# Performance work log

Hardware: AMD Instinct MI355X
Metric: run time of the kernel (lower is better)

Reference implementation:

```python
import jax, jax.numpy as jnp
import numpy as np

B, N, D, H = 32, 64, 128, 256

def setup_inputs() -> dict:
    key = jax.random.key(0)
    ks = jax.random.split(key, 6)
    s = 0.02
    return {
        "objects": jax.random.normal(ks[0], (B, N, D), dtype=jnp.float32),
        "gW1": jax.random.normal(ks[1], (2 * D, H), dtype=jnp.float32) * s,
        "gb1": jnp.zeros((H,), dtype=jnp.float32),
        "gW2": jax.random.normal(ks[2], (H, H), dtype=jnp.float32) * s,
        "gb2": jnp.zeros((H,), dtype=jnp.float32),
        "gW3": jax.random.normal(ks[3], (H, H), dtype=jnp.float32) * s,
        "gb3": jnp.zeros((H,), dtype=jnp.float32),
        "fW1": jax.random.normal(ks[4], (H, H), dtype=jnp.float32) * s,
        "fb1": jnp.zeros((H,), dtype=jnp.float32),
        "fW2": jax.random.normal(ks[5], (H, H), dtype=jnp.float32) * s,
        "fb2": jnp.zeros((H,), dtype=jnp.float32),
    }

def reference(objects, gW1, gb1, gW2, gb2, gW3, gb3, fW1, fb1, fW2, fb2):
    b, n, d = objects.shape
    # Pairwise concat: pair[b,i,j] = [objects[b,i], objects[b,j]] -> (B,N,N,2D)
    left = jnp.broadcast_to(objects[:, :, None, :], (b, n, n, d))
    right = jnp.broadcast_to(objects[:, None, :, :], (b, n, n, d))
    pair = jnp.concatenate([left, right], axis=-1)
    # g_theta: 3-layer MLP with ReLU after first two layers
    h = jax.nn.relu(pair @ gW1 + gb1)
    h = jax.nn.relu(h @ gW2 + gb2)
    h = h @ gW3 + gb3                      # (B,N,N,H)
    # Sum over all pairs i != j
    mask = (1.0 - jnp.eye(n, dtype=h.dtype))  # (N,N)
    agg = jnp.einsum('bijh,ij->bh', h, mask)  # (B,H)
    # f_phi: Linear-ReLU-Linear
    out = jax.nn.relu(agg @ fW1 + fb1) @ fW2 + fb2
    return out
```

## Files before the change

### kernel.cpp

```cpp
#include <hip/hip_runtime.h>
#include <hip/hip_bf16.h>

typedef __attribute__((ext_vector_type(8))) _Float16 half8;
typedef __attribute__((ext_vector_type(4))) float f32x4;

__global__ __launch_bounds__(256) void rn_prep(
    const float* __restrict__ obj, const float* __restrict__ gW1,
    const float* __restrict__ gb1, const float* __restrict__ gW2,
    _Float16* __restrict__ Lh, char* __restrict__ RhB,
    _Float16* __restrict__ W2h, float* __restrict__ S)
{
    __shared__ float so[8 * 128];
    __shared__ float tt[64 * 65];
    const int blk = blockIdx.x, t = threadIdx.x;

    if (blk < 256) {
        const int r0 = blk * 8;
        #pragma unroll
        for (int it = 0; it < 4; ++it) so[it * 256 + t] = obj[r0 * 128 + it * 256 + t];
        __syncthreads();
        float accL[8], accR[8];
        #pragma unroll
        for (int r = 0; r < 8; ++r) { accL[r] = 0.f; accR[r] = 0.f; }
        for (int k = 0; k < 128; ++k) {
            float wL = gW1[k * 256 + t];
            float wR = gW1[(128 + k) * 256 + t];
            #pragma unroll
            for (int r = 0; r < 8; ++r) {
                float o = so[r * 128 + k];
                accL[r] += o * wL;
                accR[r] += o * wR;
            }
        }
        float bb = gb1[t];
        #pragma unroll
        for (int r = 0; r < 8; ++r) {
            int row = r0 + r;
            Lh[row * 256 + t] = (_Float16)(accL[r] + bb);
            *(_Float16*)(RhB + row * 512 + ((2 * t) ^ ((row & 15) << 4))) = (_Float16)accR[r];
        }
    } else if (blk < 272) {
        const int tb = blk - 256;
        const int k0 = (tb >> 2) * 64, c0 = (tb & 3) * 64;
        for (int it = 0; it < 16; ++it) {
            int idx = it * 256 + t, rr = idx >> 6, cc = idx & 63;
            tt[rr * 65 + cc] = gW2[(k0 + rr) * 256 + c0 + cc];
        }
        __syncthreads();
        for (int it = 0; it < 16; ++it) {
            int idx = it * 256 + t, cr = idx >> 6, kk = idx & 63;
            W2h[(c0 + cr) * 256 + (k0 + kk)] = (_Float16)tt[kk * 65 + cr];
        }
    } else {
        for (int it = 0; it < 32; ++it) S[it * 256 + t] = 0.f;
    }
}

__global__ __launch_bounds__(512, 2) void rn_main(
    const char* __restrict__ LhB, const char* __restrict__ RhB,
    const _Float16* __restrict__ W2h, const float* __restrict__ gb2,
    float* __restrict__ S)
{
    __shared__ __attribute__((aligned(16))) char smem[36864];
    const int blk = blockIdx.x;
    const int b = blk >> 3, ig = blk & 7;
    const int t = threadIdx.x, lane = t & 63, w = t >> 6;
    const int mg = w >> 2, ng = w & 3;
    const int lc = lane & 15, lg = lane >> 4;

    {
        const char* gR = RhB + b * 32768;
        #pragma unroll
        for (int it = 0; it < 4; ++it) {
            int u = it * 512 + t;
            *(f32x4*)(smem + u * 16) = *(const f32x4*)(gR + u * 16);
        }
        if (t < 256) {
            const char* gL = LhB + (b * 64 + ig * 8) * 512;
            *(f32x4*)(smem + 32768 + t * 16) = *(const f32x4*)(gL + t * 16);
        }
    }

    half8 bfr[4][8];
    #pragma unroll
    for (int n = 0; n < 4; ++n)
        #pragma unroll
        for (int ks = 0; ks < 8; ++ks)
            bfr[n][ks] = *(const half8*)(W2h + (ng * 64 + n * 16 + lc) * 256 + ks * 32 + lg * 8);

    float bias[4];
    #pragma unroll
    for (int n = 0; n < 4; ++n) bias[n] = gb2[ng * 64 + n * 16 + lc];

    __syncthreads();

    half8 rh[2][8];
    #pragma unroll
    for (int m2 = 0; m2 < 2; ++m2) {
        int row = mg * 32 + m2 * 16 + lc;
        #pragma unroll
        for (int ks = 0; ks < 8; ++ks) {
            int kb = ks * 64 + lg * 16;
            rh[m2][ks] = *(const half8*)(smem + row * 512 + (kb ^ (lc << 4)));
        }
    }

    const half8 zero8 = {(_Float16)0.f, (_Float16)0.f, (_Float16)0.f, (_Float16)0.f,
                         (_Float16)0.f, (_Float16)0.f, (_Float16)0.f, (_Float16)0.f};
    float csum[4] = {0.f, 0.f, 0.f, 0.f};

    for (int ii = 0; ii < 8; ++ii) {
        f32x4 acc[2][4];
        #pragma unroll
        for (int m2 = 0; m2 < 2; ++m2)
            #pragma unroll
            for (int n = 0; n < 4; ++n)
                acc[m2][n] = (f32x4){0.f, 0.f, 0.f, 0.f};

        #pragma unroll
        for (int ks = 0; ks < 8; ++ks) {
            half8 lhv = *(const half8*)(smem + 32768 + ii * 512 + ks * 64 + lg * 16);
            #pragma unroll
            for (int m2 = 0; m2 < 2; ++m2) {
                half8 av = lhv + rh[m2][ks];
                av = __builtin_elementwise_max(av, zero8);
                #pragma unroll
                for (int n = 0; n < 4; ++n)
                    acc[m2][n] = __builtin_amdgcn_mfma_f32_16x16x32_f16(
                        av, bfr[n][ks], acc[m2][n], 0, 0, 0);
            }
        }

        const int iglob = ig * 8 + ii;
        #pragma unroll
        for (int n = 0; n < 4; ++n) {
            float cs = 0.f;
            #pragma unroll
            for (int m2 = 0; m2 < 2; ++m2)
                #pragma unroll
                for (int q = 0; q < 4; ++q) {
                    int row = mg * 32 + m2 * 16 + lg * 4 + q;
                    float v = fmaxf(acc[m2][n][q] + bias[n], 0.f);
                    cs += (row == iglob) ? 0.f : v;
                }
            csum[n] += cs;
        }
    }

    #pragma unroll
    for (int n = 0; n < 4; ++n) {
        float cs = csum[n];
        cs += __shfl_xor(cs, 16);
        cs += __shfl_xor(cs, 32);
        if (lane < 16) atomicAdd(&S[b * 256 + ng * 64 + n * 16 + lc], cs);
    }
}

__global__ __launch_bounds__(1024) void rn_final(
    const float* __restrict__ S, const float* __restrict__ gW3,
    const float* __restrict__ gb3, const float* __restrict__ fW1,
    const float* __restrict__ fb1, const float* __restrict__ fW2,
    const float* __restrict__ fb2, float* __restrict__ out)
{
    __shared__ float vec[256];
    __shared__ float ps[16][260];
    const int b = blockIdx.x, t = threadIdx.x;
    const int cg = t & 63, kq = t >> 6;
    const int c0 = cg * 4;

    if (t < 256) vec[t] = S[b * 256 + t];
    __syncthreads();

    {
        f32x4 s = (f32x4){0.f, 0.f, 0.f, 0.f};
        #pragma unroll
        for (int kk = 0; kk < 16; ++kk) {
            int k = kq * 16 + kk;
            f32x4 wv = *(const f32x4*)&gW3[k * 256 + c0];
            s += wv * vec[k];
        }
        *(f32x4*)&ps[kq][c0] = s;
    }
    __syncthreads();
    if (t < 256) {
        float a = 0.f;
        #pragma unroll
        for (int q = 0; q < 16; ++q) a += ps[q][t];
        vec[t] = a + 4032.0f * gb3[t];
    }
    __syncthreads();

    {
        f32x4 s = (f32x4){0.f, 0.f, 0.f, 0.f};
        #pragma unroll
        for (int kk = 0; kk < 16; ++kk) {
            int k = kq * 16 + kk;
            f32x4 wv = *(const f32x4*)&fW1[k * 256 + c0];
            s += wv * vec[k];
        }
        *(f32x4*)&ps[kq][c0] = s;
    }
    __syncthreads();
    if (t < 256) {
        float a = 0.f;
        #pragma unroll
        for (int q = 0; q < 16; ++q) a += ps[q][t];
        vec[t] = fmaxf(a + fb1[t], 0.f);
    }
    __syncthreads();

    {
        f32x4 s = (f32x4){0.f, 0.f, 0.f, 0.f};
        #pragma unroll
        for (int kk = 0; kk < 16; ++kk) {
            int k = kq * 16 + kk;
            f32x4 wv = *(const f32x4*)&fW2[k * 256 + c0];
            s += wv * vec[k];
        }
        *(f32x4*)&ps[kq][c0] = s;
    }
    __syncthreads();
    if (t < 256) {
        float a = 0.f;
        #pragma unroll
        for (int q = 0; q < 16; ++q) a += ps[q][t];
        out[b * 256 + t] = a + fb2[t];
    }
}

extern "C" void kernel_launch(void* const* d_in, const int* in_sizes, int n_in,
                              void* d_out, int out_size, void* d_ws, size_t ws_size,
                              hipStream_t stream)
{
    const float* obj = (const float*)d_in[0];
    const float* gW1 = (const float*)d_in[1];
    const float* gb1 = (const float*)d_in[2];
    const float* gW2 = (const float*)d_in[3];
    const float* gb2 = (const float*)d_in[4];
    const float* gW3 = (const float*)d_in[5];
    const float* gb3 = (const float*)d_in[6];
    const float* fW1 = (const float*)d_in[7];
    const float* fb1 = (const float*)d_in[8];
    const float* fW2 = (const float*)d_in[9];
    const float* fb2 = (const float*)d_in[10];
    float* out = (float*)d_out;

    char* ws = (char*)d_ws;
    _Float16* Lh  = (_Float16*)(ws);
    char*     RhB = ws + (1u << 20);
    _Float16* W2h = (_Float16*)(ws + (2u << 20));
    float*    S   = (float*)(ws + (2u << 20) + (128u << 10));

    rn_prep <<<273, 256, 0, stream>>>(obj, gW1, gb1, gW2, Lh, RhB, W2h, S);
    rn_main <<<256, 512, 0, stream>>>((const char*)Lh, RhB, W2h, gb2, S);
    rn_final<<<32, 1024, 0, stream>>>(S, gW3, gb3, fW1, fb1, fW2, fb2, out);
}
```

Before: 44.47 us.

## Fuse final MLP into main kernel via last-block-per-batch atomic counter

Removes the separate rn_final launch. Each rn_main block bumps a per-batch counter after its atomic adds, and the last of the 8 blocks for a batch runs the gW3/f_phi tail with 512 threads instead of 1024. The W2 fragment register loads are also hoisted ahead of the shared-memory staging to overlap global latency. This saves one kernel launch and its gap, but the tail now runs serially at the end of the last block and needs a counter reset in prep plus fences.

```diff
diff --git a/kernel.cpp b/kernel.cpp
--- a/kernel.cpp
+++ b/kernel.cpp
@@ -8,7 +8,7 @@
     const float* __restrict__ obj, const float* __restrict__ gW1,
     const float* __restrict__ gb1, const float* __restrict__ gW2,
     _Float16* __restrict__ Lh, char* __restrict__ RhB,
-    _Float16* __restrict__ W2h, float* __restrict__ S)
+    _Float16* __restrict__ W2h, float* __restrict__ S, int* __restrict__ cnt)
 {
     __shared__ float so[8 * 128];
     __shared__ float tt[64 * 65];
@@ -53,21 +53,34 @@
         }
     } else {
         for (int it = 0; it < 32; ++it) S[it * 256 + t] = 0.f;
+        if (t < 32) cnt[t] = 0;
     }
 }
 
 __global__ __launch_bounds__(512, 2) void rn_main(
     const char* __restrict__ LhB, const char* __restrict__ RhB,
     const _Float16* __restrict__ W2h, const float* __restrict__ gb2,
-    float* __restrict__ S)
+    float* __restrict__ S, int* __restrict__ cnt,
+    const float* __restrict__ gW3, const float* __restrict__ gb3,
+    const float* __restrict__ fW1, const float* __restrict__ fb1,
+    const float* __restrict__ fW2, const float* __restrict__ fb2,
+    float* __restrict__ out)
 {
     __shared__ __attribute__((aligned(16))) char smem[36864];
+    __shared__ int lastFlag;
     const int blk = blockIdx.x;
     const int b = blk >> 3, ig = blk & 7;
     const int t = threadIdx.x, lane = t & 63, w = t >> 6;
     const int mg = w >> 2, ng = w & 3;
     const int lc = lane & 15, lg = lane >> 4;
 
+    half8 bfr[4][8];
+    #pragma unroll
+    for (int n = 0; n < 4; ++n)
+        #pragma unroll
+        for (int ks = 0; ks < 8; ++ks)
+            bfr[n][ks] = *(const half8*)(W2h + (ng * 64 + n * 16 + lc) * 256 + ks * 32 + lg * 8);
+
     {
         const char* gR = RhB + b * 32768;
         #pragma unroll
@@ -80,13 +93,6 @@
             *(f32x4*)(smem + 32768 + t * 16) = *(const f32x4*)(gL + t * 16);
         }
     }
-
-    half8 bfr[4][8];
-    #pragma unroll
-    for (int n = 0; n < 4; ++n)
-        #pragma unroll
-        for (int ks = 0; ks < 8; ++ks)
-            bfr[n][ks] = *(const half8*)(W2h + (ng * 64 + n * 16 + lc) * 256 + ks * 32 + lg * 8);
 
     float bias[4];
     #pragma unroll
@@ -154,30 +160,33 @@
         cs += __shfl_xor(cs, 32);
         if (lane < 16) atomicAdd(&S[b * 256 + ng * 64 + n * 16 + lc], cs);
     }
-}
-
-__global__ __launch_bounds__(1024) void rn_final(
-    const float* __restrict__ S, const float* __restrict__ gW3,
-    const float* __restrict__ gb3, const float* __restrict__ fW1,
-    const float* __restrict__ fb1, const float* __restrict__ fW2,
-    const float* __restrict__ fb2, float* __restrict__ out)
-{
-    __shared__ float vec[256];
-    __shared__ float ps[16][260];
-    const int b = blockIdx.x, t = threadIdx.x;
+
+    __threadfence();
+    __syncthreads();
+    if (t == 0) {
+        int old = __hip_atomic_fetch_add(&cnt[b], 1, __ATOMIC_ACQ_REL,
+                                         __HIP_MEMORY_SCOPE_AGENT);
+        lastFlag = (old == 7);
+    }
+    __syncthreads();
+    if (!lastFlag) return;
+
+    float* vec = (float*)smem;
+    float (*ps)[260] = (float(*)[260])(smem + 2048);
+    if (t < 256)
+        vec[t] = __hip_atomic_load(&S[b * 256 + t], __ATOMIC_RELAXED,
+                                   __HIP_MEMORY_SCOPE_AGENT);
+    __syncthreads();
+
     const int cg = t & 63, kq = t >> 6;
     const int c0 = cg * 4;
 
-    if (t < 256) vec[t] = S[b * 256 + t];
-    __syncthreads();
-
     {
         f32x4 s = (f32x4){0.f, 0.f, 0.f, 0.f};
         #pragma unroll
-        for (int kk = 0; kk < 16; ++kk) {
-            int k = kq * 16 + kk;
-            f32x4 wv = *(const f32x4*)&gW3[k * 256 + c0];
-            s += wv * vec[k];
+        for (int kk = 0; kk < 32; ++kk) {
+            int k = kq * 32 + kk;
+            s += (*(const f32x4*)&gW3[k * 256 + c0]) * vec[k];
         }
         *(f32x4*)&ps[kq][c0] = s;
     }
@@ -185,7 +194,7 @@
     if (t < 256) {
         float a = 0.f;
         #pragma unroll
-        for (int q = 0; q < 16; ++q) a += ps[q][t];
+        for (int q = 0; q < 8; ++q) a += ps[q][t];
         vec[t] = a + 4032.0f * gb3[t];
     }
     __syncthreads();
@@ -193,10 +202,9 @@
     {
         f32x4 s = (f32x4){0.f, 0.f, 0.f, 0.f};
         #pragma unroll
-        for (int kk = 0; kk < 16; ++kk) {
-            int k = kq * 16 + kk;
-            f32x4 wv = *(const f32x4*)&fW1[k * 256 + c0];
-            s += wv * vec[k];
+        for (int kk = 0; kk < 32; ++kk) {
+            int k = kq * 32 + kk;
+            s += (*(const f32x4*)&fW1[k * 256 + c0]) * vec[k];
         }
         *(f32x4*)&ps[kq][c0] = s;
     }
@@ -204,7 +212,7 @@
     if (t < 256) {
         float a = 0.f;
         #pragma unroll
-        for (int q = 0; q < 16; ++q) a += ps[q][t];
+        for (int q = 0; q < 8; ++q) a += ps[q][t];
         vec[t] = fmaxf(a + fb1[t], 0.f);
     }
     __syncthreads();
@@ -212,10 +220,9 @@
     {
         f32x4 s = (f32x4){0.f, 0.f, 0.f, 0.f};
         #pragma unroll
-        for (int kk = 0; kk < 16; ++kk) {
-            int k = kq * 16 + kk;
-            f32x4 wv = *(const f32x4*)&fW2[k * 256 + c0];
-            s += wv * vec[k];
+        for (int kk = 0; kk < 32; ++kk) {
+            int k = kq * 32 + kk;
+            s += (*(const f32x4*)&fW2[k * 256 + c0]) * vec[k];
         }
         *(f32x4*)&ps[kq][c0] = s;
     }
@@ -223,7 +230,7 @@
     if (t < 256) {
         float a = 0.f;
         #pragma unroll
-        for (int q = 0; q < 16; ++q) a += ps[q][t];
+        for (int q = 0; q < 8; ++q) a += ps[q][t];
         out[b * 256 + t] = a + fb2[t];
     }
 }
@@ -250,8 +257,9 @@
     char*     RhB = ws + (1u << 20);
     _Float16* W2h = (_Float16*)(ws + (2u << 20));
     float*    S   = (float*)(ws + (2u << 20) + (128u << 10));
-
-    rn_prep <<<273, 256, 0, stream>>>(obj, gW1, gb1, gW2, Lh, RhB, W2h, S);
-    rn_main <<<256, 512, 0, stream>>>((const char*)Lh, RhB, W2h, gb2, S);
-    rn_final<<<32, 1024, 0, stream>>>(S, gW3, gb3, fW1, fb1, fW2, fb2, out);
+    int*      cnt = (int*)(ws + (2u << 20) + (160u << 10));
+
+    rn_prep <<<273, 256, 0, stream>>>(obj, gW1, gb1, gW2, Lh, RhB, W2h, S, cnt);
+    rn_main <<<256, 512, 0, stream>>>((const char*)Lh, RhB, W2h, gb2, S, cnt,
+                                      gW3, gb3, fW1, fb1, fW2, fb2, out);
 }
```

Result: slower. 70.94 us (+59.5%).

## Precompute gW3·fW1 product in prep kernel to drop a GEMV stage from final kernel

Applied to the files above, without the earlier changes.

The final layer gW3 and the first f_phi layer are linear back to back, so the prep kernel now builds M = gW3 @ fW1 and a folded bias vector (4032*gb3@fW1 + fb1). That lets rn_final skip one matrix-vector stage and its barriers. fW2 is also prefetched into registers early to hide its load latency. The cost is 32 extra prep blocks doing a 256x256x256 fp32 GEMM every call, plus one bias block with a serial 256-term loop. That work runs in parallel with the existing prep blocks but could lengthen the prep kernel.

```diff
diff --git a/kernel.cpp b/kernel.cpp
--- a/kernel.cpp
+++ b/kernel.cpp
@@ -7,11 +7,15 @@
 __global__ __launch_bounds__(256) void rn_prep(
     const float* __restrict__ obj, const float* __restrict__ gW1,
     const float* __restrict__ gb1, const float* __restrict__ gW2,
+    const float* __restrict__ gW3, const float* __restrict__ gb3,
+    const float* __restrict__ fW1, const float* __restrict__ fb1,
     _Float16* __restrict__ Lh, char* __restrict__ RhB,
-    _Float16* __restrict__ W2h, float* __restrict__ S)
+    _Float16* __restrict__ W2h, float* __restrict__ S,
+    float* __restrict__ M, float* __restrict__ dvec)
 {
     __shared__ float so[8 * 128];
     __shared__ float tt[64 * 65];
+    __shared__ float sg[8][256];
     const int blk = blockIdx.x, t = threadIdx.x;
 
     if (blk < 256) {
@@ -51,8 +55,26 @@
             int idx = it * 256 + t, cr = idx >> 6, kk = idx & 63;
             W2h[(c0 + cr) * 256 + (k0 + kk)] = (_Float16)tt[kk * 65 + cr];
         }
+    } else if (blk == 272) {
+        for (int it = 0; it < 32; ++it) S[it * 256 + t] = 0.f;
+        float a = 0.f;
+        for (int j = 0; j < 256; ++j) a += gb3[j] * fW1[j * 256 + t];
+        dvec[t] = 4032.0f * a + fb1[t];
     } else {
-        for (int it = 0; it < 32; ++it) S[it * 256 + t] = 0.f;
+        const int r0 = (blk - 273) * 8;
+        #pragma unroll
+        for (int it = 0; it < 8; ++it) sg[it][t] = gW3[(r0 + it) * 256 + t];
+        __syncthreads();
+        float acc[8];
+        #pragma unroll
+        for (int r = 0; r < 8; ++r) acc[r] = 0.f;
+        for (int j = 0; j < 256; ++j) {
+            float wv = fW1[j * 256 + t];
+            #pragma unroll
+            for (int r = 0; r < 8; ++r) acc[r] += sg[r][j] * wv;
+        }
+        #pragma unroll
+        for (int r = 0; r < 8; ++r) M[(r0 + r) * 256 + t] = acc[r];
     }
 }
 
@@ -157,9 +179,8 @@
 }
 
 __global__ __launch_bounds__(1024) void rn_final(
-    const float* __restrict__ S, const float* __restrict__ gW3,
-    const float* __restrict__ gb3, const float* __restrict__ fW1,
-    const float* __restrict__ fb1, const float* __restrict__ fW2,
+    const float* __restrict__ S, const float* __restrict__ M,
+    const float* __restrict__ dvec, const float* __restrict__ fW2,
     const float* __restrict__ fb2, float* __restrict__ out)
 {
     __shared__ float vec[256];
@@ -171,52 +192,33 @@
     if (t < 256) vec[t] = S[b * 256 + t];
     __syncthreads();
 
+    f32x4 w2r[16];
     {
         f32x4 s = (f32x4){0.f, 0.f, 0.f, 0.f};
         #pragma unroll
         for (int kk = 0; kk < 16; ++kk) {
             int k = kq * 16 + kk;
-            f32x4 wv = *(const f32x4*)&gW3[k * 256 + c0];
-            s += wv * vec[k];
+            s += (*(const f32x4*)&M[k * 256 + c0]) * vec[k];
         }
         *(f32x4*)&ps[kq][c0] = s;
+        #pragma unroll
+        for (int kk = 0; kk < 16; ++kk)
+            w2r[kk] = *(const f32x4*)&fW2[(kq * 16 + kk) * 256 + c0];
     }
     __syncthreads();
     if (t < 256) {
         float a = 0.f;
         #pragma unroll
         for (int q = 0; q < 16; ++q) a += ps[q][t];
-        vec[t] = a + 4032.0f * gb3[t];
+        vec[t] = fmaxf(a + dvec[t], 0.f);
     }
     __syncthreads();
 
     {
         f32x4 s = (f32x4){0.f, 0.f, 0.f, 0.f};
         #pragma unroll
-        for (int kk = 0; kk < 16; ++kk) {
-            int k = kq * 16 + kk;
-            f32x4 wv = *(const f32x4*)&fW1[k * 256 + c0];
-            s += wv * vec[k];
-        }
-        *(f32x4*)&ps[kq][c0] = s;
-    }
-    __syncthreads();
-    if (t < 256) {
-        float a = 0.f;
-        #pragma unroll
-        for (int q = 0; q < 16; ++q) a += ps[q][t];
-        vec[t] = fmaxf(a + fb1[t], 0.f);
-    }
-    __syncthreads();
-
-    {
-        f32x4 s = (f32x4){0.f, 0.f, 0.f, 0.f};
-        #pragma unroll
-        for (int kk = 0; kk < 16; ++kk) {
-            int k = kq * 16 + kk;
-            f32x4 wv = *(const f32x4*)&fW2[k * 256 + c0];
-            s += wv * vec[k];
-        }
+        for (int kk = 0; kk < 16; ++kk)
+            s += w2r[kk] * vec[kq * 16 + kk];
         *(f32x4*)&ps[kq][c0] = s;
     }
     __syncthreads();
@@ -250,8 +252,11 @@
     char*     RhB = ws + (1u << 20);
     _Float16* W2h = (_Float16*)(ws + (2u << 20));
     float*    S   = (float*)(ws + (2u << 20) + (128u << 10));
-
-    rn_prep <<<273, 256, 0, stream>>>(obj, gW1, gb1, gW2, Lh, RhB, W2h, S);
+    float*    M   = (float*)(ws + (2u << 20) + (160u << 10));
+    float*    dv  = (float*)(ws + (2u << 20) + (416u << 10));
+
+    rn_prep <<<305, 256, 0, stream>>>(obj, gW1, gb1, gW2, gW3, gb3, fW1, fb1,
+                                      Lh, RhB, W2h, S, M, dv);
     rn_main <<<256, 512, 0, stream>>>((const char*)Lh, RhB, W2h, gb2, S);
-    rn_final<<<32, 1024, 0, stream>>>(S, gW3, gb3, fW1, fb1, fW2, fb2, out);
-}
+    rn_final<<<32, 1024, 0, stream>>>(S, M, dv, fW2, fb2, out);
+}
```

Result: slower. 47.95 us (+7.8%).

## Split rn_main output columns across two blocks with 1024 threads each

Applied to the files above, without the earlier changes.

Reworks the main pairwise kernel so each block handles half of the 256 output columns, with 16 waves each owning one 16-row tile and two 16-column tiles. The grid doubles to 512 blocks of 1024 threads, cutting per-thread register state (fewer B fragments and accumulators) and giving more waves to hide latency. The cost is that each block still loads the full R tile and L rows, so shared-memory fill traffic doubles, and the ReLU-add of the A operand is now recomputed per column half. The rn_final edits are cosmetic.

```diff
diff --git a/kernel.cpp b/kernel.cpp
--- a/kernel.cpp
+++ b/kernel.cpp
@@ -56,23 +56,35 @@
     }
 }
 
-__global__ __launch_bounds__(512, 2) void rn_main(
+__global__ __launch_bounds__(1024) void rn_main(
     const char* __restrict__ LhB, const char* __restrict__ RhB,
     const _Float16* __restrict__ W2h, const float* __restrict__ gb2,
     float* __restrict__ S)
 {
     __shared__ __attribute__((aligned(16))) char smem[36864];
     const int blk = blockIdx.x;
-    const int b = blk >> 3, ig = blk & 7;
+    const int b = blk >> 4, ig = (blk >> 1) & 7, half = blk & 1;
     const int t = threadIdx.x, lane = t & 63, w = t >> 6;
-    const int mg = w >> 2, ng = w & 3;
+    const int mr = w & 3, nc = w >> 2;
     const int lc = lane & 15, lg = lane >> 4;
 
+    half8 bfr[2][8];
+    #pragma unroll
+    for (int n = 0; n < 2; ++n)
+        #pragma unroll
+        for (int ks = 0; ks < 8; ++ks)
+            bfr[n][ks] = *(const half8*)(W2h +
+                (half * 128 + nc * 32 + n * 16 + lc) * 256 + ks * 32 + lg * 8);
+
+    float bias[2];
+    #pragma unroll
+    for (int n = 0; n < 2; ++n) bias[n] = gb2[half * 128 + nc * 32 + n * 16 + lc];
+
     {
         const char* gR = RhB + b * 32768;
         #pragma unroll
-        for (int it = 0; it < 4; ++it) {
-            int u = it * 512 + t;
+        for (int it = 0; it < 2; ++it) {
+            int u = it * 1024 + t;
             *(f32x4*)(smem + u * 16) = *(const f32x4*)(gR + u * 16);
         }
         if (t < 256) {
@@ -80,79 +92,53 @@
             *(f32x4*)(smem + 32768 + t * 16) = *(const f32x4*)(gL + t * 16);
         }
     }
-
-    half8 bfr[4][8];
-    #pragma unroll
-    for (int n = 0; n < 4; ++n)
-        #pragma unroll
-        for (int ks = 0; ks < 8; ++ks)
-            bfr[n][ks] = *(const half8*)(W2h + (ng * 64 + n * 16 + lc) * 256 + ks * 32 + lg * 8);
-
-    float bias[4];
-    #pragma unroll
-    for (int n = 0; n < 4; ++n) bias[n] = gb2[ng * 64 + n * 16 + lc];
-
-    __syncthreads();
-
-    half8 rh[2][8];
-    #pragma unroll
-    for (int m2 = 0; m2 < 2; ++m2) {
-        int row = mg * 32 + m2 * 16 + lc;
+    __syncthreads();
+
+    half8 rh[8];
+    {
+        int row = mr * 16 + lc;
         #pragma unroll
         for (int ks = 0; ks < 8; ++ks) {
             int kb = ks * 64 + lg * 16;
-            rh[m2][ks] = *(const half8*)(smem + row * 512 + (kb ^ (lc << 4)));
+            rh[ks] = *(const half8*)(smem + row * 512 + (kb ^ (lc << 4)));
         }
     }
 
     const half8 zero8 = {(_Float16)0.f, (_Float16)0.f, (_Float16)0.f, (_Float16)0.f,
                          (_Float16)0.f, (_Float16)0.f, (_Float16)0.f, (_Float16)0.f};
-    float csum[4] = {0.f, 0.f, 0.f, 0.f};
-
+    float csum[2] = {0.f, 0.f};
+
+    #pragma unroll 1
     for (int ii = 0; ii < 8; ++ii) {
-        f32x4 acc[2][4];
-        #pragma unroll
-        for (int m2 = 0; m2 < 2; ++m2)
-            #pragma unroll
-            for (int n = 0; n < 4; ++n)
-                acc[m2][n] = (f32x4){0.f, 0.f, 0.f, 0.f};
+        f32x4 acc0 = (f32x4){0.f, 0.f, 0.f, 0.f};
+        f32x4 acc1 = (f32x4){0.f, 0.f, 0.f, 0.f};
 
         #pragma unroll
         for (int ks = 0; ks < 8; ++ks) {
             half8 lhv = *(const half8*)(smem + 32768 + ii * 512 + ks * 64 + lg * 16);
-            #pragma unroll
-            for (int m2 = 0; m2 < 2; ++m2) {
-                half8 av = lhv + rh[m2][ks];
-                av = __builtin_elementwise_max(av, zero8);
-                #pragma unroll
-                for (int n = 0; n < 4; ++n)
-                    acc[m2][n] = __builtin_amdgcn_mfma_f32_16x16x32_f16(
-                        av, bfr[n][ks], acc[m2][n], 0, 0, 0);
-            }
+            half8 av = __builtin_elementwise_max(lhv + rh[ks], zero8);
+            acc0 = __builtin_amdgcn_mfma_f32_16x16x32_f16(av, bfr[0][ks], acc0, 0, 0, 0);
+            acc1 = __builtin_amdgcn_mfma_f32_16x16x32_f16(av, bfr[1][ks], acc1, 0, 0, 0);
         }
 
         const int iglob = ig * 8 + ii;
         #pragma unroll
-        for (int n = 0; n < 4; ++n) {
-            float cs = 0.f;
-            #pragma unroll
-            for (int m2 = 0; m2 < 2; ++m2)
-                #pragma unroll
-                for (int q = 0; q < 4; ++q) {
-                    int row = mg * 32 + m2 * 16 + lg * 4 + q;
-                    float v = fmaxf(acc[m2][n][q] + bias[n], 0.f);
-                    cs += (row == iglob) ? 0.f : v;
-                }
-            csum[n] += cs;
+        for (int q = 0; q < 4; ++q) {
+            int row = mr * 16 + lg * 4 + q;
+            float v0 = fmaxf(acc0[q] + bias[0], 0.f);
+            float v1 = fmaxf(acc1[q] + bias[1], 0.f);
+            csum[0] += (row == iglob) ? 0.f : v0;
+            csum[1] += (row == iglob) ? 0.f : v1;
         }
     }
 
     #pragma unroll
-    for (int n = 0; n < 4; ++n) {
+    for (int n = 0; n < 2; ++n) {
         float cs = csum[n];
         cs += __shfl_xor(cs, 16);
         cs += __shfl_xor(cs, 32);
-        if (lane < 16) atomicAdd(&S[b * 256 + ng * 64 + n * 16 + lc], cs);
+        if (lane < 16)
+            atomicAdd(&S[b * 256 + half * 128 + nc * 32 + n * 16 + lc], cs);
     }
 }
 
@@ -176,8 +162,7 @@
         #pragma unroll
         for (int kk = 0; kk < 16; ++kk) {
             int k = kq * 16 + kk;
-            f32x4 wv = *(const f32x4*)&gW3[k * 256 + c0];
-            s += wv * vec[k];
+            s += (*(const f32x4*)&gW3[k * 256 + c0]) * vec[k];
         }
         *(f32x4*)&ps[kq][c0] = s;
     }
@@ -195,8 +180,7 @@
         #pragma unroll
         for (int kk = 0; kk < 16; ++kk) {
             int k = kq * 16 + kk;
-            f32x4 wv = *(const f32x4*)&fW1[k * 256 + c0];
-            s += wv * vec[k];
+            s += (*(const f32x4*)&fW1[k * 256 + c0]) * vec[k];
         }
         *(f32x4*)&ps[kq][c0] = s;
     }
@@ -214,8 +198,7 @@
         #pragma unroll
         for (int kk = 0; kk < 16; ++kk) {
             int k = kq * 16 + kk;
-            f32x4 wv = *(const f32x4*)&fW2[k * 256 + c0];
-            s += wv * vec[k];
+            s += (*(const f32x4*)&fW2[k * 256 + c0]) * vec[k];
         }
         *(f32x4*)&ps[kq][c0] = s;
     }
@@ -252,6 +235,6 @@
     float*    S   = (float*)(ws + (2u << 20) + (128u << 10));
 
     rn_prep <<<273, 256, 0, stream>>>(obj, gW1, gb1, gW2, Lh, RhB, W2h, S);
-    rn_main <<<256, 512, 0, stream>>>((const char*)Lh, RhB, W2h, gb2, S);
+    rn_main <<<512, 1024, 0, stream>>>((const char*)Lh, RhB, W2h, gb2, S);
     rn_final<<<32, 1024, 0, stream>>>(S, gW3, gb3, fW1, fb1, fW2, fb2, out);
 }
```

New measurement: 55.05 us. 1.24x slower.
